# Kernel optimization log

Hardware: AMD Instinct MI355X
Metric: run time of the kernel (lower is better)

## Reference

```python
import jax, jax.numpy as jnp
import numpy as np

N_HEADS = 12   # hard-coded in Attention.__init__
HEAD_DIM = 64  # hard-coded in Attention.__init__


def setup_inputs() -> dict:
    key = jax.random.key(0)
    ks = jax.random.split(key, 6)
    S, B, D = 512, 8, 1024
    NB = 8
    BD = D // NB                 # 128
    E = N_HEADS * HEAD_DIM       # 768
    sc = 0.02
    return {
        'x':       jax.random.normal(ks[0], (S, B, D), jnp.float32),
        'w_comp':  jax.random.normal(ks[1], (NB, BD, 1), jnp.float32) * 0.05,
        'wq':      jax.random.normal(ks[2], (NB, BD, E), jnp.float32) * sc,
        'wk':      jax.random.normal(ks[3], (NB, BD, E), jnp.float32) * sc,
        'wv':      jax.random.normal(ks[4], (NB, BD, E), jnp.float32) * sc,
        'w_final': jax.random.normal(ks[5], (NB, E, BD), jnp.float32) * sc,
    }


def reference(x, w_comp, wq, wk, wv, w_final):
    S, B, D = x.shape
    NB, BD, E = wq.shape
    nh, hd = N_HEADS, HEAD_DIM
    scale = hd ** (-0.5)

    xb = x.reshape(S, B, NB, BD)  # split into blocks

    # competition-based block gating: GroupLinear(block_dim -> 1) + softmax over blocks
    comp_logits = jnp.einsum('sbnd,ndo->sbno', xb, w_comp)[..., 0]  # [S,B,NB]
    comp = jax.nn.softmax(comp_logits, axis=2)
    xg = xb * comp[..., None]

    # block-wise GroupLinear QKV projections -> [S,B,NB,nh,hd]
    q = jnp.einsum('sbnd,nde->sbne', xg, wq).reshape(S, B, NB, nh, hd)
    k = jnp.einsum('sbnd,nde->sbne', xg, wk).reshape(S, B, NB, nh, hd)
    v = jnp.einsum('sbnd,nde->sbne', xg, wv).reshape(S, B, NB, nh, hd)

    # transpose(2,3): heads before blocks -> attention over the block axis
    q = jnp.swapaxes(q, 2, 3) * scale  # [S,B,nh,NB,hd]
    k = jnp.swapaxes(k, 2, 3)
    v = jnp.swapaxes(v, 2, 3)

    score = jnp.einsum('sbhnd,sbhmd->sbhnm', q, k)  # [S,B,nh,NB,NB]
    attn = jax.nn.softmax(score, axis=-1)
    out = jnp.einsum('sbhnm,sbhmd->sbhnd', attn, v)  # [S,B,nh,NB,hd]

    out = jnp.swapaxes(out, 2, 3).reshape(S, B, NB, nh * hd)
    out = jnp.einsum('sbne,ned->sbnd', out, w_final).reshape(S, B, D)

    score_mean = attn.mean(axis=2)  # mean over heads -> [S,B,NB,NB]
    return out, score_mean
```

## Files before the change

kernel.cpp:

```cpp
#include <hip/hip_runtime.h>
#include <hip/hip_bf16.h>

typedef __bf16 bf16;
typedef __bf16 bf16x8 __attribute__((ext_vector_type(8)));
typedef float f32x4 __attribute__((ext_vector_type(4)));

#define S_TOK 4096
#define D_DIM 1024
#define NBLK 8
#define BDIM 128
#define E_DIM 768
#define NH 12
#define HD 64
#define QKVW 2304

__global__ __launch_bounds__(256) void prep_weights(
    const float* __restrict__ wq, const float* __restrict__ wk,
    const float* __restrict__ wv, const float* __restrict__ wfin,
    bf16* __restrict__ wcatT, bf16* __restrict__ wfinT) {
  long idx = (long)blockIdx.x * 256 + threadIdx.x;
  const long NCAT = (long)NBLK * QKVW * BDIM;
  if (idx < NCAT) {
    int k = idx & (BDIM - 1);
    long rem = idx >> 7;
    int j = (int)(rem % QKVW);
    int n = (int)(rem / QKVW);
    const float* src; int jj;
    if (j < 768) { src = wq; jj = j; }
    else if (j < 1536) { src = wk; jj = j - 768; }
    else { src = wv; jj = j - 1536; }
    float v = src[((long)n * BDIM + k) * E_DIM + jj];
    wcatT[idx] = (bf16)v;
  } else {
    long i2 = idx - NCAT;
    if (i2 < (long)NBLK * BDIM * E_DIM) {
      int e = (int)(i2 % E_DIM);
      long rem = i2 / E_DIM;
      int d = (int)(rem & (BDIM - 1));
      int n = (int)(rem >> 7);
      float v = wfin[((long)n * E_DIM + e) * BDIM + d];
      wfinT[i2] = (bf16)v;
    }
  }
}

__global__ __launch_bounds__(256) void gate_kernel(
    const float* __restrict__ x, const float* __restrict__ wcomp,
    bf16* __restrict__ xg) {
  int tok = blockIdx.x;
  int t = threadIdx.x;
  int n = t >> 5;
  int l = t & 31;
  const float* xrow = x + (long)tok * D_DIM + n * BDIM;
  float xv[4]; float part = 0.f;
#pragma unroll
  for (int i = 0; i < 4; ++i) {
    int d = l + i * 32;
    xv[i] = xrow[d];
    part += xv[i] * wcomp[n * BDIM + d];
  }
#pragma unroll
  for (int m = 16; m >= 1; m >>= 1) part += __shfl_xor(part, m, 64);
  __shared__ float logits[NBLK];
  __shared__ float comp[NBLK];
  if (l == 0) logits[n] = part;
  __syncthreads();
  if (t == 0) {
    float mx = logits[0];
#pragma unroll
    for (int i = 1; i < 8; ++i) mx = fmaxf(mx, logits[i]);
    float s = 0.f, e[8];
#pragma unroll
    for (int i = 0; i < 8; ++i) { e[i] = __expf(logits[i] - mx); s += e[i]; }
    float inv = 1.f / s;
#pragma unroll
    for (int i = 0; i < 8; ++i) comp[i] = e[i] * inv;
  }
  __syncthreads();
  float c = comp[n];
  bf16* dst = xg + ((long)n * S_TOK + tok) * BDIM;
#pragma unroll
  for (int i = 0; i < 4; ++i) dst[l + i * 32] = (bf16)(xv[i] * c);
}

__device__ __forceinline__ void stage_tile(char* lds, const char* g, long rstride) {
  int wave = threadIdx.x >> 6, lane = threadIdx.x & 63;
#pragma unroll
  for (int s = 0; s < 8; ++s) {
    int instr = wave * 8 + s;
    int row = instr * 4 + (lane >> 4);
    int chunk = (lane & 15) ^ (row & 7);
    const char* src = g + (long)row * rstride + chunk * 16;
    __builtin_amdgcn_global_load_lds(
        (const __attribute__((address_space(1))) void*)src,
        (__attribute__((address_space(3))) void*)(lds + instr * 1024), 16, 0, 0);
  }
}

__device__ __forceinline__ bf16x8 ld_frag(const char* lds, int row, int kchunk) {
  int chunk = kchunk ^ (row & 7);
  return *(const bf16x8*)(lds + row * 256 + chunk * 16);
}

__device__ __forceinline__ void mfma_slab(const char* ldsA, const char* ldsB,
                                          f32x4 acc[4][4], int wm, int wn, int lane) {
#pragma unroll
  for (int ks = 0; ks < 4; ++ks) {
    int kchunk = ks * 4 + (lane >> 4);
    bf16x8 af[4], bfr[4];
#pragma unroll
    for (int i = 0; i < 4; ++i) af[i] = ld_frag(ldsA, wm + i * 16 + (lane & 15), kchunk);
#pragma unroll
    for (int j = 0; j < 4; ++j) bfr[j] = ld_frag(ldsB, wn + j * 16 + (lane & 15), kchunk);
#pragma unroll
    for (int i = 0; i < 4; ++i)
#pragma unroll
      for (int j = 0; j < 4; ++j)
        acc[i][j] = __builtin_amdgcn_mfma_f32_16x16x32_bf16(af[i], bfr[j], acc[i][j], 0, 0, 0);
  }
}

__global__ __launch_bounds__(256) void qkv_gemm(
    const bf16* __restrict__ xg, const bf16* __restrict__ wcatT,
    bf16* __restrict__ qkv, int t0) {
  __shared__ char ldsA[32768];
  __shared__ char ldsB[32768];
  int nt = blockIdx.x;
  int mt = blockIdx.y;
  int blk = blockIdx.z;
  const char* Ab = (const char*)(xg + ((long)blk * S_TOK + t0 + mt * 128) * BDIM);
  const char* Bb = (const char*)(wcatT + ((long)blk * QKVW + nt * 128) * BDIM);
  stage_tile(ldsA, Ab, 256);
  stage_tile(ldsB, Bb, 256);
  __syncthreads();
  int wave = threadIdx.x >> 6, lane = threadIdx.x & 63;
  int wm = (wave >> 1) * 64, wn = (wave & 1) * 64;
  f32x4 acc[4][4] = {};
  mfma_slab(ldsA, ldsB, acc, wm, wn, lane);
  int rbase = (lane >> 4) * 4;
  int cb = lane & 15;
  long tokl0 = (long)mt * 128;
#pragma unroll
  for (int i = 0; i < 4; ++i) {
#pragma unroll
    for (int r = 0; r < 4; ++r) {
      long tokl = tokl0 + wm + i * 16 + rbase + r;
      bf16* dst = qkv + tokl * (NBLK * QKVW) + (long)blk * QKVW + nt * 128 + wn + cb;
#pragma unroll
      for (int j = 0; j < 4; ++j) dst[j * 16] = (bf16)acc[i][j][r];
    }
  }
}

__device__ __forceinline__ int4 shfl4(int4 v, int src) {
  int4 r;
  r.x = __shfl(v.x, src, 64); r.y = __shfl(v.y, src, 64);
  r.z = __shfl(v.z, src, 64); r.w = __shfl(v.w, src, 64);
  return r;
}

__global__ __launch_bounds__(256) void attn_kernel(
    const bf16* __restrict__ qkv, bf16* __restrict__ attn_out,
    float* __restrict__ out2, int t0) {
  __shared__ float smp[4][64];
  int t = threadIdx.x;
  int wave = t >> 6, lane = t & 63;
  int tl = blockIdx.x;
  long tok = t0 + tl;
  int n = lane >> 3, c = lane & 7;
  const bf16* base = qkv + (long)tl * (NBLK * QKVW) + n * QKVW + c * 8;
  float smacc[8] = {};
#pragma unroll
  for (int hi = 0; hi < 3; ++hi) {
    int h = wave + hi * 4;
    const bf16* hb = base + h * HD;
    int4 q4 = *(const int4*)(hb);
    int4 k4 = *(const int4*)(hb + E_DIM);
    int4 v4 = *(const int4*)(hb + 2 * E_DIM);
    bf16x8 q8 = __builtin_bit_cast(bf16x8, q4);
    float qf[8];
#pragma unroll
    for (int u = 0; u < 8; ++u) qf[u] = (float)q8[u];
    float sp[8];
#pragma unroll
    for (int m = 0; m < 8; ++m) {
      bf16x8 km = __builtin_bit_cast(bf16x8, shfl4(k4, m * 8 + c));
      float acc = 0.f;
#pragma unroll
      for (int u = 0; u < 8; ++u) acc += qf[u] * (float)km[u];
      sp[m] = acc;
    }
#pragma unroll
    for (int m = 0; m < 8; ++m) {
#pragma unroll
      for (int msk = 1; msk < 8; msk <<= 1) sp[m] += __shfl_xor(sp[m], msk, 64);
      sp[m] *= 0.125f;
    }
    float mx = sp[0];
#pragma unroll
    for (int m = 1; m < 8; ++m) mx = fmaxf(mx, sp[m]);
    float a[8]; float ssum = 0.f;
#pragma unroll
    for (int m = 0; m < 8; ++m) { a[m] = __expf(sp[m] - mx); ssum += a[m]; }
    float inv = 1.f / ssum;
#pragma unroll
    for (int m = 0; m < 8; ++m) { a[m] *= inv; smacc[m] += a[m]; }
    float of[8] = {};
#pragma unroll
    for (int m = 0; m < 8; ++m) {
      bf16x8 vm = __builtin_bit_cast(bf16x8, shfl4(v4, m * 8 + c));
#pragma unroll
      for (int u = 0; u < 8; ++u) of[u] += a[m] * (float)vm[u];
    }
    bf16x8 ov;
#pragma unroll
    for (int u = 0; u < 8; ++u) ov[u] = (bf16)of[u];
    *(int4*)(attn_out + ((long)n * S_TOK + tok) * E_DIM + h * HD + c * 8) =
        __builtin_bit_cast(int4, ov);
  }
  float sel = smacc[0];
#pragma unroll
  for (int m = 1; m < 8; ++m) if (c == m) sel = smacc[m];
  smp[wave][lane] = sel;
  __syncthreads();
  if (t < 64) {
    float v = (smp[0][t] + smp[1][t] + smp[2][t] + smp[3][t]) * (1.f / 12.f);
    out2[tok * 64 + t] = v;
  }
}

__global__ __launch_bounds__(256) void final_gemm(
    const bf16* __restrict__ attn_out, const bf16* __restrict__ wfinT,
    float* __restrict__ out) {
  __shared__ char ldsA[32768];
  __shared__ char ldsB[32768];
  int mt = blockIdx.y;
  int blk = blockIdx.z;
  int wave = threadIdx.x >> 6, lane = threadIdx.x & 63;
  int wm = (wave >> 1) * 64, wn = (wave & 1) * 64;
  f32x4 acc[4][4] = {};
  const char* Abase = (const char*)(attn_out + ((long)blk * S_TOK + mt * 128) * E_DIM);
  const char* Bbase = (const char*)(wfinT + (long)blk * BDIM * E_DIM);
  for (int kt = 0; kt < 6; ++kt) {
    stage_tile(ldsA, Abase + kt * 256, E_DIM * 2);
    stage_tile(ldsB, Bbase + kt * 256, E_DIM * 2);
    __syncthreads();
    mfma_slab(ldsA, ldsB, acc, wm, wn, lane);
    __syncthreads();
  }
  int rbase = (lane >> 4) * 4;
  int cb = lane & 15;
#pragma unroll
  for (int i = 0; i < 4; ++i) {
#pragma unroll
    for (int r = 0; r < 4; ++r) {
      long tok = (long)mt * 128 + wm + i * 16 + rbase + r;
      float* dst = out + tok * D_DIM + blk * BDIM + wn + cb;
#pragma unroll
      for (int j = 0; j < 4; ++j) dst[j * 16] = acc[i][j][r];
    }
  }
}

extern "C" void kernel_launch(void* const* d_in, const int* in_sizes, int n_in,
                              void* d_out, int out_size, void* d_ws, size_t ws_size,
                              hipStream_t stream) {
  const float* x     = (const float*)d_in[0];
  const float* wcomp = (const float*)d_in[1];
  const float* wq    = (const float*)d_in[2];
  const float* wk    = (const float*)d_in[3];
  const float* wv    = (const float*)d_in[4];
  const float* wfin  = (const float*)d_in[5];
  float* out  = (float*)d_out;
  float* out2 = out + (long)S_TOK * D_DIM;

  char* ws = (char*)d_ws;
  bf16* xg    = (bf16*)ws;
  bf16* wcatT = (bf16*)(ws + 8388608);
  bf16* wfinT = (bf16*)(ws + 8388608 + 4718592);
  const long FIXED = 14680064;
  bf16* attnb = (bf16*)(ws + FIXED);
  const long ATTNB = 50331648;
  char* dyn = ws + FIXED + ATTNB;
  long avail = (long)ws_size - (FIXED + ATTNB);
  long TC = avail > 0 ? avail / 36864 : 0;
  if (TC > 2048) TC = 2048;
  TC &= ~127L;
  if (TC < 128) TC = 128;
  bf16* qkvb = (bf16*)dyn;

  prep_weights<<<12288, 256, 0, stream>>>(wq, wk, wv, wfin, wcatT, wfinT);
  gate_kernel<<<S_TOK, 256, 0, stream>>>(x, wcomp, xg);
  for (int t0 = 0; t0 < S_TOK; t0 += (int)TC) {
    int tc = S_TOK - t0; if (tc > TC) tc = (int)TC;
    dim3 g2(18, tc / 128, 8);
    qkv_gemm<<<g2, 256, 0, stream>>>(xg, wcatT, qkvb, t0);
    attn_kernel<<<tc, 256, 0, stream>>>(qkvb, attnb, out2, t0);
  }
  dim3 g4(1, 32, 8);
  final_gemm<<<g4, 256, 0, stream>>>(attnb, wfinT, out);
}
```

Baseline: 220.9 us.

## Stage QKV epilogue through LDS, double-buffer final GEMM, enlarge token chunk

The QKV GEMM epilogue now writes its accumulator tile to LDS and then emits coalesced 16-byte global stores, replacing scattered 2-byte stores. The final GEMM double-buffers its LDS tiles so the next K-slab loads while MFMAs run on the current one, at the cost of 128KB of LDS per block and lower occupancy. The token chunk cap is raised to the full sequence, cutting the number of qkv/attn launch pairs when the workspace allows, at the cost of a larger intermediate buffer.

New measurement: 210.7 us. -4.6%, faster.

```diff
diff --git a/kernel.cpp b/kernel.cpp
--- a/kernel.cpp
+++ b/kernel.cpp
@@ -137,18 +137,28 @@
   int wm = (wave >> 1) * 64, wn = (wave & 1) * 64;
   f32x4 acc[4][4] = {};
   mfma_slab(ldsA, ldsB, acc, wm, wn, lane);
+  __syncthreads();
+  bf16* cst = (bf16*)ldsA;
   int rbase = (lane >> 4) * 4;
   int cb = lane & 15;
+#pragma unroll
+  for (int i = 0; i < 4; ++i)
+#pragma unroll
+    for (int j = 0; j < 4; ++j) {
+      int col = wn + j * 16 + cb;
+#pragma unroll
+      for (int r = 0; r < 4; ++r)
+        cst[(wm + i * 16 + rbase + r) * 128 + col] = (bf16)acc[i][j][r];
+    }
+  __syncthreads();
+  int rr = threadIdx.x >> 4;
+  int co = (threadIdx.x & 15) * 8;
   long tokl0 = (long)mt * 128;
 #pragma unroll
-  for (int i = 0; i < 4; ++i) {
-#pragma unroll
-    for (int r = 0; r < 4; ++r) {
-      long tokl = tokl0 + wm + i * 16 + rbase + r;
-      bf16* dst = qkv + tokl * (NBLK * QKVW) + (long)blk * QKVW + nt * 128 + wn + cb;
-#pragma unroll
-      for (int j = 0; j < 4; ++j) dst[j * 16] = (bf16)acc[i][j][r];
-    }
+  for (int p = 0; p < 8; ++p) {
+    int row = rr + p * 16;
+    bf16* dst = qkv + (tokl0 + row) * (NBLK * QKVW) + (long)blk * QKVW + nt * 128 + co;
+    *(int4*)dst = *(const int4*)(cst + row * 128 + co);
   }
 }
 
@@ -232,8 +242,8 @@
 __global__ __launch_bounds__(256) void final_gemm(
     const bf16* __restrict__ attn_out, const bf16* __restrict__ wfinT,
     float* __restrict__ out) {
-  __shared__ char ldsA[32768];
-  __shared__ char ldsB[32768];
+  __shared__ char ldsA[2][32768];
+  __shared__ char ldsB[2][32768];
   int mt = blockIdx.y;
   int blk = blockIdx.z;
   int wave = threadIdx.x >> 6, lane = threadIdx.x & 63;
@@ -241,13 +251,18 @@
   f32x4 acc[4][4] = {};
   const char* Abase = (const char*)(attn_out + ((long)blk * S_TOK + mt * 128) * E_DIM);
   const char* Bbase = (const char*)(wfinT + (long)blk * BDIM * E_DIM);
-  for (int kt = 0; kt < 6; ++kt) {
-    stage_tile(ldsA, Abase + kt * 256, E_DIM * 2);
-    stage_tile(ldsB, Bbase + kt * 256, E_DIM * 2);
+  stage_tile(ldsA[0], Abase, E_DIM * 2);
+  stage_tile(ldsB[0], Bbase, E_DIM * 2);
+  __syncthreads();
+  int cur = 0;
+  for (int kt = 0; kt < 5; ++kt) {
+    stage_tile(ldsA[cur ^ 1], Abase + (kt + 1) * 256, E_DIM * 2);
+    stage_tile(ldsB[cur ^ 1], Bbase + (kt + 1) * 256, E_DIM * 2);
+    mfma_slab(ldsA[cur], ldsB[cur], acc, wm, wn, lane);
     __syncthreads();
-    mfma_slab(ldsA, ldsB, acc, wm, wn, lane);
-    __syncthreads();
-  }
+    cur ^= 1;
+  }
+  mfma_slab(ldsA[cur], ldsB[cur], acc, wm, wn, lane);
   int rbase = (lane >> 4) * 4;
   int cb = lane & 15;
 #pragma unroll
@@ -284,7 +299,7 @@
   char* dyn = ws + FIXED + ATTNB;
   long avail = (long)ws_size - (FIXED + ATTNB);
   long TC = avail > 0 ? avail / 36864 : 0;
-  if (TC > 2048) TC = 2048;
+  if (TC > S_TOK) TC = S_TOK;
   TC &= ~127L;
   if (TC < 128) TC = 128;
   bf16* qkvb = (bf16*)dyn;
```
